# Optimization experiments

Measured on AMD Instinct MI355X. Metric: run time of the kernel, lower is better.

The kernel has to match this reference:

```python
import jax, jax.numpy as jnp
import numpy as np

T, B, OBS, A, P, NB, H = 32, 256, 1024, 16, 600, 601, 128


def setup_inputs() -> dict:
    key = jax.random.key(0)
    ks = jax.random.split(key, 32)
    f32 = jnp.float32

    def rn(k, shape, scale):
        return jax.random.normal(k, shape, dtype=f32) * scale

    hh = 1.0 / np.sqrt(H)
    inp = {
        "obs_seq": rn(ks[0], (T, B, OBS), 1.0),
        # backbone MLP (512, 512)
        "bb_w1": rn(ks[1], (OBS, 512), 1.0 / np.sqrt(OBS)), "bb_b1": jnp.zeros((512,), f32),
        "bb_w2": rn(ks[2], (512, 512), 1.0 / np.sqrt(512)), "bb_b2": jnp.zeros((512,), f32),
        # feedforward heads (final layers init std=0.01, bias 0 per module)
        "pol_w": rn(ks[3], (512, A), 0.01), "pol_b": jnp.zeros((A,), f32),
        "y_w": rn(ks[4], (512, P), 0.01), "y_b": jnp.zeros((P,), f32),
        "ci_w": rn(ks[5], (512, H), 1.0 / np.sqrt(512)), "ci_b": jnp.zeros((H,), f32),
        # LSTMCell(A, 128): gate order i,f,g,o as in torch
        "w_ih": rn(ks[6], (A, 4 * H), hh), "w_hh": rn(ks[7], (H, 4 * H), hh),
        "b_ih": rn(ks[8], (4 * H,), hh), "b_hh": rn(ks[9], (4 * H,), hh),
        # z / q / aux_pi MLPs: Linear(128,128) -> ReLU -> Linear(128, out)
        "z_w1": rn(ks[10], (H, H), hh), "z_b1": jnp.zeros((H,), f32),
        "z_w2": rn(ks[11], (H, P), 0.01), "z_b2": jnp.zeros((P,), f32),
        "q_w1": rn(ks[12], (H, H), hh), "q_b1": jnp.zeros((H,), f32),
        "q_w2": rn(ks[13], (H, NB), 0.01), "q_b2": jnp.zeros((NB,), f32),
        "a_w1": rn(ks[14], (H, H), hh), "a_b1": jnp.zeros((H,), f32),
        "a_w2": rn(ks[15], (H, A), 0.01), "a_b2": jnp.zeros((A,), f32),
    }
    return inp


def reference(obs_seq, bb_w1, bb_b1, bb_w2, bb_b2, pol_w, pol_b, y_w, y_b,
              ci_w, ci_b, w_ih, w_hh, b_ih, b_hh,
              z_w1, z_b1, z_w2, z_b2, q_w1, q_b1, q_w2, q_b2,
              a_w1, a_b1, a_w2, a_b2):
    Tn, Bn = obs_seq.shape[:2]
    x = obs_seq.reshape(Tn * Bn, -1)  # feedforward across time: fold T into batch
    emb = jax.nn.relu(jax.nn.relu(x @ bb_w1 + bb_b1) @ bb_w2 + bb_b2)  # [N,512]
    logits = emb @ pol_w + pol_b  # [N,A]
    y = emb @ y_w + y_b           # [N,P]
    c0 = emb @ ci_w + ci_b        # [N,H]
    h0 = jnp.tanh(c0)

    # one_hot(a) @ W_ih^T == row a of W_ih (input-to-gate contribution per action)
    in_gates = w_ih + b_ih  # [A, 4H]

    def step(carry, ig):
        h, c = carry
        g = ig + h @ w_hh + b_hh  # [N,4H]
        i, f, gg, o = jnp.split(g, 4, axis=-1)  # torch gate order i,f,g,o
        c = jax.nn.sigmoid(f) * c + jax.nn.sigmoid(i) * jnp.tanh(gg)
        h = jax.nn.sigmoid(o) * jnp.tanh(c)
        return (h, c), h

    _, h_all = jax.lax.scan(step, (h0, c0), in_gates)  # [A, N, H]

    def mlp(hx, w1, b1, w2, b2):
        return jax.nn.relu(hx @ w1 + b1) @ w2 + b2

    def to_tba(arr):
        Aa, N, D = arr.shape
        return arr.reshape(Aa, Tn, Bn, D).transpose(1, 2, 0, 3)  # [T,B,A,D]

    z = to_tba(mlp(h_all, z_w1, z_b1, z_w2, z_b2))
    q = to_tba(mlp(h_all, q_w1, q_b1, q_w2, q_b2))
    aux_pi = to_tba(mlp(h_all, a_w1, a_b1, a_w2, a_b2))
    return (logits.reshape(Tn, Bn, -1), y.reshape(Tn, Bn, -1), z, q, aux_pi)
```

## Files before the change

### kernel.cpp

```cpp
#include <hip/hip_runtime.h>
#include <stdint.h>

typedef short bf16x8 __attribute__((ext_vector_type(8)));
typedef float f32x4 __attribute__((ext_vector_type(4)));

__device__ __forceinline__ unsigned short f2b(float f) {
  union { float f; unsigned u; } v; v.f = f;
  unsigned r = v.u + 0x7fffu + ((v.u >> 16) & 1u);
  return (unsigned short)(r >> 16);
}

struct TD { const float* in; unsigned short* out; int R, C; };
struct TDs { TD d[12]; };

__global__ __launch_bounds__(256) void tconv_all(TDs ds) {
  TD t = ds.d[blockIdx.z];
  int c0 = blockIdx.x * 32, r0 = blockIdx.y * 32;
  if (c0 >= t.C || r0 >= t.R) return;
  __shared__ float tl[32][33];
  int tx = threadIdx.x & 31, ty = threadIdx.x >> 5;
  #pragma unroll
  for (int i = 0; i < 32; i += 8) {
    int r = r0 + ty + i, c = c0 + tx;
    tl[ty + i][tx] = (r < t.R && c < t.C) ? t.in[(size_t)r * t.C + c] : 0.f;
  }
  __syncthreads();
  #pragma unroll
  for (int i = 0; i < 32; i += 8) {
    int c = c0 + ty + i, r = r0 + tx;
    if (c < t.C && r < t.R) t.out[(size_t)c * t.R + r] = f2b(tl[tx][ty + i]);
  }
}

__global__ __launch_bounds__(256) void conv_k(const float* __restrict__ in,
                                              unsigned short* __restrict__ out, int n) {
  int i = (blockIdx.x * 256 + threadIdx.x) * 8;
  if (i >= n) return;
  float4 a = *(const float4*)(in + i);
  float4 b = *(const float4*)(in + i + 4);
  bf16x8 v;
  v[0] = (short)f2b(a.x); v[1] = (short)f2b(a.y); v[2] = (short)f2b(a.z); v[3] = (short)f2b(a.w);
  v[4] = (short)f2b(b.x); v[5] = (short)f2b(b.y); v[6] = (short)f2b(b.z); v[7] = (short)f2b(b.w);
  *(bf16x8*)(out + i) = v;
}

template <int ACT, bool OBF16>
__global__ __launch_bounds__(256) void gemm_k(const unsigned short* __restrict__ A,
                                              const unsigned short* __restrict__ BT,
                                              const float* __restrict__ bias,
                                              void* __restrict__ Cp,
                                              int M, int N, int K, int ldC) {
  __shared__ unsigned short As[64][40];
  __shared__ unsigned short Bs[64][40];
  const int tid = threadIdx.x;
  const int n0 = blockIdx.x * 64;
  const int m0 = blockIdx.y * 64;
  const int wid = tid >> 6, lane = tid & 63;
  const int wm = (wid >> 1) * 32, wn = (wid & 1) * 32;
  const int lr = lane & 15, lk = lane >> 4;
  const int sr = tid >> 2, sc = (tid & 3) * 8;

  f32x4 acc[2][2] = {};

  for (int k0 = 0; k0 < K; k0 += 32) {
    *(bf16x8*)&As[sr][sc] = *(const bf16x8*)(A + (size_t)(m0 + sr) * K + k0 + sc);
    {
      int n = n0 + sr;
      bf16x8 v = {};
      if (n < N) v = *(const bf16x8*)(BT + (size_t)n * K + k0 + sc);
      *(bf16x8*)&Bs[sr][sc] = v;
    }
    __syncthreads();
    bf16x8 af[2], bfr[2];
    #pragma unroll
    for (int mi = 0; mi < 2; mi++) af[mi] = *(const bf16x8*)&As[wm + mi * 16 + lr][lk * 8];
    #pragma unroll
    for (int ni = 0; ni < 2; ni++) bfr[ni] = *(const bf16x8*)&Bs[wn + ni * 16 + lr][lk * 8];
    #pragma unroll
    for (int mi = 0; mi < 2; mi++)
      #pragma unroll
      for (int ni = 0; ni < 2; ni++)
        acc[mi][ni] = __builtin_amdgcn_mfma_f32_16x16x32_bf16(af[mi], bfr[ni], acc[mi][ni], 0, 0, 0);
    __syncthreads();
  }

  #pragma unroll
  for (int mi = 0; mi < 2; mi++)
    #pragma unroll
    for (int ni = 0; ni < 2; ni++) {
      int col = n0 + wn + ni * 16 + lr;
      if (col >= N) continue;
      float bv = bias[col];
      #pragma unroll
      for (int r = 0; r < 4; r++) {
        int row = m0 + wm + mi * 16 + lk * 4 + r;
        float v = acc[mi][ni][r] + bv;
        if (ACT == 1) v = fmaxf(v, 0.f);
        if (OBF16) ((unsigned short*)Cp)[(size_t)row * ldC + col] = f2b(v);
        else       ((float*)Cp)[(size_t)row * ldC + col] = v;
      }
    }
}

__global__ __launch_bounds__(256) void lstm_k(const float* __restrict__ c0,
                                              const unsigned short* __restrict__ whhT,
                                              const float* __restrict__ w_ih,
                                              const float* __restrict__ b_ih,
                                              const float* __restrict__ b_hh,
                                              unsigned short* __restrict__ h_all) {
  __shared__ float G[32][516];
  __shared__ float cst[32][128];
  __shared__ unsigned short hst[32][136];
  const int tid = threadIdx.x, lane = tid & 63, wid = tid >> 6;
  const int r0 = blockIdx.x * 32;
  const int lr = lane & 15, lk = lane >> 4;

  for (int e = tid; e < 32 * 128; e += 256) {
    int r = e >> 7, j = e & 127;
    float c = c0[(size_t)(r0 + r) * 128 + j];
    cst[r][j] = c;
    hst[r][j] = f2b(tanhf(c));
  }
  __syncthreads();

  for (int a = 0; a < 16; a++) {
    f32x4 acc[2][8] = {};
    #pragma unroll
    for (int ks = 0; ks < 4; ks++) {
      bf16x8 af0 = *(const bf16x8*)&hst[lr][ks * 32 + lk * 8];
      bf16x8 af1 = *(const bf16x8*)&hst[16 + lr][ks * 32 + lk * 8];
      #pragma unroll
      for (int ni = 0; ni < 8; ni++) {
        int col = wid * 128 + ni * 16 + lr;
        bf16x8 bv = *(const bf16x8*)(whhT + (size_t)col * 128 + ks * 32 + lk * 8);
        acc[0][ni] = __builtin_amdgcn_mfma_f32_16x16x32_bf16(af0, bv, acc[0][ni], 0, 0, 0);
        acc[1][ni] = __builtin_amdgcn_mfma_f32_16x16x32_bf16(af1, bv, acc[1][ni], 0, 0, 0);
      }
    }
    #pragma unroll
    for (int mi = 0; mi < 2; mi++)
      #pragma unroll
      for (int ni = 0; ni < 8; ni++)
        #pragma unroll
        for (int rr = 0; rr < 4; rr++)
          G[mi * 16 + lk * 4 + rr][wid * 128 + ni * 16 + lr] = acc[mi][ni][rr];
    __syncthreads();

    const float* ig = w_ih + a * 512;
    for (int e = tid; e < 32 * 128; e += 256) {
      int r = e >> 7, j = e & 127;
      float gi = G[r][j]       + ig[j]       + b_ih[j]       + b_hh[j];
      float gf = G[r][j + 128] + ig[j + 128] + b_ih[j + 128] + b_hh[j + 128];
      float gg = G[r][j + 256] + ig[j + 256] + b_ih[j + 256] + b_hh[j + 256];
      float go = G[r][j + 384] + ig[j + 384] + b_ih[j + 384] + b_hh[j + 384];
      float c = cst[r][j];
      float si = 1.f / (1.f + __expf(-gi));
      float sf = 1.f / (1.f + __expf(-gf));
      float so = 1.f / (1.f + __expf(-go));
      float cn = sf * c + si * tanhf(gg);
      float h = so * tanhf(cn);
      cst[r][j] = cn;
      unsigned short hb = f2b(h);
      hst[r][j] = hb;
      h_all[((size_t)(r0 + r) * 16 + a) * 128 + j] = hb;
    }
    __syncthreads();
  }
}

__global__ __launch_bounds__(256) void heads_k(
    const unsigned short* __restrict__ hall,
    const unsigned short* __restrict__ zw1, const float* __restrict__ zb1,
    const unsigned short* __restrict__ zw2, const float* __restrict__ zb2,
    const unsigned short* __restrict__ qw1, const float* __restrict__ qb1,
    const unsigned short* __restrict__ qw2, const float* __restrict__ qb2,
    const unsigned short* __restrict__ aw1, const float* __restrict__ ab1,
    const unsigned short* __restrict__ aw2, const float* __restrict__ ab2,
    float* __restrict__ oz, float* __restrict__ oq, float* __restrict__ oa) {
  __shared__ unsigned short hs[64][136];
  __shared__ unsigned short hd[64][136];
  const int tid = threadIdx.x;
  const int r0 = blockIdx.x * 64;
  const int lane = tid & 63, wid = tid >> 6;
  const int lr = lane & 15, lk = lane >> 4;

  {
    int row = tid >> 2, cb = (tid & 3) * 8;
    #pragma unroll
    for (int it = 0; it < 4; it++) {
      int col = cb + it * 32;
      *(bf16x8*)&hs[row][col] = *(const bf16x8*)(hall + (size_t)(r0 + row) * 128 + col);
    }
  }
  __syncthreads();

  const unsigned short* W1[3] = {zw1, qw1, aw1};
  const float*          B1[3] = {zb1, qb1, ab1};
  const unsigned short* W2[3] = {zw2, qw2, aw2};
  const float*          B2[3] = {zb2, qb2, ab2};
  float*                OO[3] = {oz, oq, oa};
  const int             NN[3] = {600, 601, 16};

  #pragma unroll
  for (int hi = 0; hi < 3; hi++) {
    const unsigned short* w1 = W1[hi];
    const unsigned short* w2 = W2[hi];
    const float* b1 = B1[hi];
    const float* b2 = B2[hi];
    float* Oh = OO[hi];
    const int Nh = NN[hi];

    {
      bf16x8 ha[4][4];
      #pragma unroll
      for (int mi = 0; mi < 4; mi++)
        #pragma unroll
        for (int ks = 0; ks < 4; ks++)
          ha[mi][ks] = *(const bf16x8*)&hs[mi * 16 + lr][ks * 32 + lk * 8];
      f32x4 hacc[4][2] = {};
      #pragma unroll
      for (int ks = 0; ks < 4; ks++)
        #pragma unroll
        for (int nj = 0; nj < 2; nj++) {
          int col = wid * 32 + nj * 16 + lr;
          bf16x8 bv = *(const bf16x8*)(w1 + (size_t)col * 128 + ks * 32 + lk * 8);
          #pragma unroll
          for (int mi = 0; mi < 4; mi++)
            hacc[mi][nj] = __builtin_amdgcn_mfma_f32_16x16x32_bf16(ha[mi][ks], bv, hacc[mi][nj], 0, 0, 0);
        }
      #pragma unroll
      for (int mi = 0; mi < 4; mi++)
        #pragma unroll
        for (int nj = 0; nj < 2; nj++) {
          int col = wid * 32 + nj * 16 + lr;
          float bb = b1[col];
          #pragma unroll
          for (int rr = 0; rr < 4; rr++) {
            int row = mi * 16 + lk * 4 + rr;
            hd[row][col] = f2b(fmaxf(hacc[mi][nj][rr] + bb, 0.f));
          }
        }
    }
    __syncthreads();

    {
      bf16x8 hda[4][4];
      #pragma unroll
      for (int mi = 0; mi < 4; mi++)
        #pragma unroll
        for (int ks = 0; ks < 4; ks++)
          hda[mi][ks] = *(const bf16x8*)&hd[mi * 16 + lr][ks * 32 + lk * 8];

      const int NF = (Nh + 15) >> 4;
      const int fpw = (NF + 3) >> 2;
      const int f0 = wid * fpw;
      const int f1 = min(NF, f0 + fpw);

      for (int f = f0; f < f1; f += 2) {
        f32x4 oacc[4][2] = {};
        #pragma unroll
        for (int ks = 0; ks < 4; ks++)
          #pragma unroll
          for (int nj = 0; nj < 2; nj++) {
            int nf = f + nj; nf = nf < f1 ? nf : f1 - 1;
            int col = nf * 16 + lr;
            int bc = col < Nh ? col : Nh - 1;
            bf16x8 bv = *(const bf16x8*)(w2 + (size_t)bc * 128 + ks * 32 + lk * 8);
            #pragma unroll
            for (int mi = 0; mi < 4; mi++)
              oacc[mi][nj] = __builtin_amdgcn_mfma_f32_16x16x32_bf16(hda[mi][ks], bv, oacc[mi][nj], 0, 0, 0);
          }
        #pragma unroll
        for (int nj = 0; nj < 2; nj++) {
          int nf = f + nj;
          if (nf >= f1) break;
          int col = nf * 16 + lr;
          if (col < Nh) {
            float bb = b2[col];
            #pragma unroll
            for (int mi = 0; mi < 4; mi++)
              #pragma unroll
              for (int rr = 0; rr < 4; rr++) {
                int row = r0 + mi * 16 + lk * 4 + rr;
                Oh[(size_t)row * Nh + col] = oacc[mi][nj][rr] + bb;
              }
          }
        }
      }
    }
    __syncthreads();
  }
}

extern "C" void kernel_launch(void* const* d_in, const int* in_sizes, int n_in,
                              void* d_out, int out_size, void* d_ws, size_t ws_size,
                              hipStream_t stream) {
  const float* obs   = (const float*)d_in[0];
  const float* bb_w1 = (const float*)d_in[1];
  const float* bb_b1 = (const float*)d_in[2];
  const float* bb_w2 = (const float*)d_in[3];
  const float* bb_b2 = (const float*)d_in[4];
  const float* pol_w = (const float*)d_in[5];
  const float* pol_b = (const float*)d_in[6];
  const float* y_w   = (const float*)d_in[7];
  const float* y_b   = (const float*)d_in[8];
  const float* ci_w  = (const float*)d_in[9];
  const float* ci_b  = (const float*)d_in[10];
  const float* w_ih  = (const float*)d_in[11];
  const float* w_hh  = (const float*)d_in[12];
  const float* b_ih  = (const float*)d_in[13];
  const float* b_hh  = (const float*)d_in[14];
  const float* z_w1  = (const float*)d_in[15];
  const float* z_b1  = (const float*)d_in[16];
  const float* z_w2  = (const float*)d_in[17];
  const float* z_b2  = (const float*)d_in[18];
  const float* q_w1  = (const float*)d_in[19];
  const float* q_b1  = (const float*)d_in[20];
  const float* q_w2  = (const float*)d_in[21];
  const float* q_b2  = (const float*)d_in[22];
  const float* a_w1  = (const float*)d_in[23];
  const float* a_b1  = (const float*)d_in[24];
  const float* a_w2  = (const float*)d_in[25];
  const float* a_b2  = (const float*)d_in[26];

  float* out = (float*)d_out;
  float* out_logits = out;
  float* out_y      = out + 131072;
  float* out_z      = out + 5046272;
  float* out_q      = out + 83689472;
  float* out_a      = out + 162463744;

  uint8_t* ws = (uint8_t*)d_ws;
  size_t off = 0;
  auto alc = [&](size_t bytes) -> void* {
    void* p = ws + off;
    off = (off + bytes + 255) & ~(size_t)255;
    return p;
  };
  unsigned short* W1T  = (unsigned short*)alc((size_t)512 * 1024 * 2);
  unsigned short* W2T  = (unsigned short*)alc((size_t)512 * 512 * 2);
  unsigned short* polT = (unsigned short*)alc((size_t)16 * 512 * 2);
  unsigned short* yT   = (unsigned short*)alc((size_t)600 * 512 * 2);
  unsigned short* ciT  = (unsigned short*)alc((size_t)128 * 512 * 2);
  unsigned short* whhT = (unsigned short*)alc((size_t)512 * 128 * 2);
  unsigned short* zw1T = (unsigned short*)alc((size_t)128 * 128 * 2);
  unsigned short* zw2T = (unsigned short*)alc((size_t)600 * 128 * 2);
  unsigned short* qw1T = (unsigned short*)alc((size_t)128 * 128 * 2);
  unsigned short* qw2T = (unsigned short*)alc((size_t)601 * 128 * 2);
  unsigned short* aw1T = (unsigned short*)alc((size_t)128 * 128 * 2);
  unsigned short* aw2T = (unsigned short*)alc((size_t)16 * 128 * 2);
  unsigned short* obsb = (unsigned short*)alc((size_t)8192 * 1024 * 2);
  unsigned short* hid1 = (unsigned short*)alc((size_t)8192 * 512 * 2);
  unsigned short* emb  = (unsigned short*)alc((size_t)8192 * 512 * 2);
  float*          c0b  = (float*)alc((size_t)8192 * 128 * 4);
  unsigned short* hall = (unsigned short*)alc((size_t)8192 * 16 * 128 * 2);
  (void)ws_size; (void)in_sizes; (void)n_in; (void)out_size;

  dim3 B256(256);

  TDs td;
  td.d[0]  = {bb_w1, W1T, 1024, 512};
  td.d[1]  = {bb_w2, W2T, 512, 512};
  td.d[2]  = {pol_w, polT, 512, 16};
  td.d[3]  = {y_w,   yT,   512, 600};
  td.d[4]  = {ci_w,  ciT,  512, 128};
  td.d[5]  = {w_hh,  whhT, 128, 512};
  td.d[6]  = {z_w1,  zw1T, 128, 128};
  td.d[7]  = {z_w2,  zw2T, 128, 600};
  td.d[8]  = {q_w1,  qw1T, 128, 128};
  td.d[9]  = {q_w2,  qw2T, 128, 601};
  td.d[10] = {a_w1,  aw1T, 128, 128};
  td.d[11] = {a_w2,  aw2T, 128, 16};
  tconv_all<<<dim3(19, 32, 12), B256, 0, stream>>>(td);

  conv_k<<<dim3(4096), B256, 0, stream>>>(obs, obsb, 8192 * 1024);

  gemm_k<1, true><<<dim3(8, 128), B256, 0, stream>>>(obsb, W1T, bb_b1, hid1, 8192, 512, 1024, 512);
  gemm_k<1, true><<<dim3(8, 128), B256, 0, stream>>>(hid1, W2T, bb_b2, emb,  8192, 512, 512,  512);
  gemm_k<0, false><<<dim3(1, 128),  B256, 0, stream>>>(emb, polT, pol_b, out_logits, 8192, 16,  512, 16);
  gemm_k<0, false><<<dim3(10, 128), B256, 0, stream>>>(emb, yT,   y_b,   out_y,      8192, 600, 512, 600);
  gemm_k<0, false><<<dim3(2, 128),  B256, 0, stream>>>(emb, ciT,  ci_b,  c0b,        8192, 128, 512, 128);
  lstm_k<<<dim3(256), B256, 0, stream>>>(c0b, whhT, w_ih, b_ih, b_hh, hall);
  heads_k<<<dim3(2048), B256, 0, stream>>>(hall,
                                           zw1T, z_b1, zw2T, z_b2,
                                           qw1T, q_b1, qw2T, q_b2,
                                           aw1T, a_b1, aw2T, a_b2,
                                           out_z, out_q, out_a);
}
```

Before: 523.2 us.

## Widen LSTM blocks, fuse head first layers, use nontemporal output stores

```diff
diff --git a/kernel.cpp b/kernel.cpp
--- a/kernel.cpp
+++ b/kernel.cpp
@@ -3,11 +3,18 @@
 
 typedef short bf16x8 __attribute__((ext_vector_type(8)));
 typedef float f32x4 __attribute__((ext_vector_type(4)));
+typedef unsigned short u16x4 __attribute__((ext_vector_type(4)));
 
 __device__ __forceinline__ unsigned short f2b(float f) {
   union { float f; unsigned u; } v; v.f = f;
   unsigned r = v.u + 0x7fffu + ((v.u >> 16) & 1u);
   return (unsigned short)(r >> 16);
+}
+__device__ __forceinline__ float fsigm(float x) { return 1.f / (1.f + __expf(-x)); }
+__device__ __forceinline__ float ftanh(float x) {
+  float t = __expf(-2.f * fabsf(x));
+  float r = (1.f - t) / (1.f + t);
+  return copysignf(r, x);
 }
 
 struct TD { const float* in; unsigned short* out; int R, C; };
@@ -44,7 +51,7 @@
   *(bf16x8*)(out + i) = v;
 }
 
-template <int ACT, bool OBF16>
+template <int ACT, bool OBF16, bool NT>
 __global__ __launch_bounds__(256) void gemm_k(const unsigned short* __restrict__ A,
                                               const unsigned short* __restrict__ BT,
                                               const float* __restrict__ bias,
@@ -97,17 +104,18 @@
         float v = acc[mi][ni][r] + bv;
         if (ACT == 1) v = fmaxf(v, 0.f);
         if (OBF16) ((unsigned short*)Cp)[(size_t)row * ldC + col] = f2b(v);
+        else if (NT) __builtin_nontemporal_store(v, (float*)Cp + (size_t)row * ldC + col);
         else       ((float*)Cp)[(size_t)row * ldC + col] = v;
       }
     }
 }
 
-__global__ __launch_bounds__(256) void lstm_k(const float* __restrict__ c0,
-                                              const unsigned short* __restrict__ whhT,
-                                              const float* __restrict__ w_ih,
-                                              const float* __restrict__ b_ih,
-                                              const float* __restrict__ b_hh,
-                                              unsigned short* __restrict__ h_all) {
+__global__ __launch_bounds__(1024) void lstm_k(const float* __restrict__ c0,
+                                               const unsigned short* __restrict__ whhT,
+                                               const float* __restrict__ w_ih,
+                                               const float* __restrict__ b_ih,
+                                               const float* __restrict__ b_hh,
+                                               unsigned short* __restrict__ h_all) {
   __shared__ float G[32][516];
   __shared__ float cst[32][128];
   __shared__ unsigned short hst[32][136];
@@ -115,50 +123,52 @@
   const int r0 = blockIdx.x * 32;
   const int lr = lane & 15, lk = lane >> 4;
 
-  for (int e = tid; e < 32 * 128; e += 256) {
-    int r = e >> 7, j = e & 127;
-    float c = c0[(size_t)(r0 + r) * 128 + j];
-    cst[r][j] = c;
-    hst[r][j] = f2b(tanhf(c));
+  {
+    int r = tid >> 5, j4 = (tid & 31) * 4;
+    float4 c4 = *(const float4*)(c0 + (size_t)(r0 + r) * 128 + j4);
+    *(f32x4*)&cst[r][j4] = f32x4{c4.x, c4.y, c4.z, c4.w};
+    u16x4 h4;
+    h4[0] = f2b(ftanh(c4.x)); h4[1] = f2b(ftanh(c4.y));
+    h4[2] = f2b(ftanh(c4.z)); h4[3] = f2b(ftanh(c4.w));
+    *(u16x4*)&hst[r][j4] = h4;
   }
   __syncthreads();
 
   for (int a = 0; a < 16; a++) {
-    f32x4 acc[2][8] = {};
+    f32x4 acc[2][2] = {};
     #pragma unroll
     for (int ks = 0; ks < 4; ks++) {
       bf16x8 af0 = *(const bf16x8*)&hst[lr][ks * 32 + lk * 8];
       bf16x8 af1 = *(const bf16x8*)&hst[16 + lr][ks * 32 + lk * 8];
       #pragma unroll
-      for (int ni = 0; ni < 8; ni++) {
-        int col = wid * 128 + ni * 16 + lr;
+      for (int nj = 0; nj < 2; nj++) {
+        int col = wid * 32 + nj * 16 + lr;
         bf16x8 bv = *(const bf16x8*)(whhT + (size_t)col * 128 + ks * 32 + lk * 8);
-        acc[0][ni] = __builtin_amdgcn_mfma_f32_16x16x32_bf16(af0, bv, acc[0][ni], 0, 0, 0);
-        acc[1][ni] = __builtin_amdgcn_mfma_f32_16x16x32_bf16(af1, bv, acc[1][ni], 0, 0, 0);
+        acc[0][nj] = __builtin_amdgcn_mfma_f32_16x16x32_bf16(af0, bv, acc[0][nj], 0, 0, 0);
+        acc[1][nj] = __builtin_amdgcn_mfma_f32_16x16x32_bf16(af1, bv, acc[1][nj], 0, 0, 0);
       }
     }
     #pragma unroll
     for (int mi = 0; mi < 2; mi++)
       #pragma unroll
-      for (int ni = 0; ni < 8; ni++)
+      for (int nj = 0; nj < 2; nj++)
         #pragma unroll
         for (int rr = 0; rr < 4; rr++)
-          G[mi * 16 + lk * 4 + rr][wid * 128 + ni * 16 + lr] = acc[mi][ni][rr];
+          G[mi * 16 + lk * 4 + rr][wid * 32 + nj * 16 + lr] = acc[mi][nj][rr];
     __syncthreads();
 
     const float* ig = w_ih + a * 512;
-    for (int e = tid; e < 32 * 128; e += 256) {
+    #pragma unroll
+    for (int it = 0; it < 4; it++) {
+      int e = tid + it * 1024;
       int r = e >> 7, j = e & 127;
       float gi = G[r][j]       + ig[j]       + b_ih[j]       + b_hh[j];
       float gf = G[r][j + 128] + ig[j + 128] + b_ih[j + 128] + b_hh[j + 128];
       float gg = G[r][j + 256] + ig[j + 256] + b_ih[j + 256] + b_hh[j + 256];
       float go = G[r][j + 384] + ig[j + 384] + b_ih[j + 384] + b_hh[j + 384];
       float c = cst[r][j];
-      float si = 1.f / (1.f + __expf(-gi));
-      float sf = 1.f / (1.f + __expf(-gf));
-      float so = 1.f / (1.f + __expf(-go));
-      float cn = sf * c + si * tanhf(gg);
-      float h = so * tanhf(cn);
+      float cn = fsigm(gf) * c + fsigm(gi) * ftanh(gg);
+      float h = fsigm(go) * ftanh(cn);
       cst[r][j] = cn;
       unsigned short hb = f2b(h);
       hst[r][j] = hb;
@@ -170,15 +180,13 @@
 
 __global__ __launch_bounds__(256) void heads_k(
     const unsigned short* __restrict__ hall,
-    const unsigned short* __restrict__ zw1, const float* __restrict__ zb1,
-    const unsigned short* __restrict__ zw2, const float* __restrict__ zb2,
-    const unsigned short* __restrict__ qw1, const float* __restrict__ qb1,
-    const unsigned short* __restrict__ qw2, const float* __restrict__ qb2,
-    const unsigned short* __restrict__ aw1, const float* __restrict__ ab1,
-    const unsigned short* __restrict__ aw2, const float* __restrict__ ab2,
+    const unsigned short* __restrict__ w1cat,
+    const float* __restrict__ zb1, const float* __restrict__ qb1, const float* __restrict__ ab1,
+    const unsigned short* __restrict__ w2cat,
+    const float* __restrict__ zb2, const float* __restrict__ qb2, const float* __restrict__ ab2,
     float* __restrict__ oz, float* __restrict__ oq, float* __restrict__ oa) {
   __shared__ unsigned short hs[64][136];
-  __shared__ unsigned short hd[64][136];
+  __shared__ unsigned short hd[64][392];
   const int tid = threadIdx.x;
   const int r0 = blockIdx.x * 64;
   const int lane = tid & 63, wid = tid >> 6;
@@ -194,101 +202,75 @@
   }
   __syncthreads();
 
-  const unsigned short* W1[3] = {zw1, qw1, aw1};
-  const float*          B1[3] = {zb1, qb1, ab1};
-  const unsigned short* W2[3] = {zw2, qw2, aw2};
-  const float*          B2[3] = {zb2, qb2, ab2};
-  float*                OO[3] = {oz, oq, oa};
-  const int             NN[3] = {600, 601, 16};
+  {
+    bf16x8 ha[4][4];
+    #pragma unroll
+    for (int mi = 0; mi < 4; mi++)
+      #pragma unroll
+      for (int ks = 0; ks < 4; ks++)
+        ha[mi][ks] = *(const bf16x8*)&hs[mi * 16 + lr][ks * 32 + lk * 8];
+    #pragma unroll
+    for (int j = 0; j < 6; j++) {
+      int nf = wid * 6 + j;
+      int col = nf * 16 + lr;
+      bf16x8 bv[4];
+      #pragma unroll
+      for (int ks = 0; ks < 4; ks++)
+        bv[ks] = *(const bf16x8*)(w1cat + (size_t)col * 128 + ks * 32 + lk * 8);
+      f32x4 hacc[4] = {};
+      #pragma unroll
+      for (int ks = 0; ks < 4; ks++)
+        #pragma unroll
+        for (int mi = 0; mi < 4; mi++)
+          hacc[mi] = __builtin_amdgcn_mfma_f32_16x16x32_bf16(ha[mi][ks], bv[ks], hacc[mi], 0, 0, 0);
+      float bb = (col < 128) ? zb1[col] : (col < 256) ? qb1[col - 128] : ab1[col - 256];
+      #pragma unroll
+      for (int mi = 0; mi < 4; mi++)
+        #pragma unroll
+        for (int rr = 0; rr < 4; rr++)
+          hd[mi * 16 + lk * 4 + rr][col] = f2b(fmaxf(hacc[mi][rr] + bb, 0.f));
+    }
+  }
+  __syncthreads();
 
   #pragma unroll
   for (int hi = 0; hi < 3; hi++) {
-    const unsigned short* w1 = W1[hi];
-    const unsigned short* w2 = W2[hi];
-    const float* b1 = B1[hi];
-    const float* b2 = B2[hi];
-    float* Oh = OO[hi];
-    const int Nh = NN[hi];
-
-    {
-      bf16x8 ha[4][4];
-      #pragma unroll
-      for (int mi = 0; mi < 4; mi++)
-        #pragma unroll
-        for (int ks = 0; ks < 4; ks++)
-          ha[mi][ks] = *(const bf16x8*)&hs[mi * 16 + lr][ks * 32 + lk * 8];
-      f32x4 hacc[4][2] = {};
-      #pragma unroll
-      for (int ks = 0; ks < 4; ks++)
-        #pragma unroll
-        for (int nj = 0; nj < 2; nj++) {
-          int col = wid * 32 + nj * 16 + lr;
-          bf16x8 bv = *(const bf16x8*)(w1 + (size_t)col * 128 + ks * 32 + lk * 8);
+    const int NF = (hi == 0) ? 38 : (hi == 1) ? 38 : 1;
+    const int Nh = (hi == 0) ? 600 : (hi == 1) ? 601 : 16;
+    const int so = (hi == 0) ? 0 : (hi == 1) ? 600 : 1201;
+    const float* b2 = (hi == 0) ? zb2 : (hi == 1) ? qb2 : ab2;
+    float* Oh = (hi == 0) ? oz : (hi == 1) ? oq : oa;
+
+    bf16x8 hda[4][4];
+    #pragma unroll
+    for (int mi = 0; mi < 4; mi++)
+      #pragma unroll
+      for (int ks = 0; ks < 4; ks++)
+        hda[mi][ks] = *(const bf16x8*)&hd[mi * 16 + lr][hi * 128 + ks * 32 + lk * 8];
+
+    for (int f = wid; f < NF; f += 4) {
+      int col = f * 16 + lr;
+      int bc = col < Nh ? col : Nh - 1;
+      bf16x8 bv[4];
+      #pragma unroll
+      for (int ks = 0; ks < 4; ks++)
+        bv[ks] = *(const bf16x8*)(w2cat + (size_t)(so + bc) * 128 + ks * 32 + lk * 8);
+      f32x4 oacc[4] = {};
+      #pragma unroll
+      for (int ks = 0; ks < 4; ks++)
+        #pragma unroll
+        for (int mi = 0; mi < 4; mi++)
+          oacc[mi] = __builtin_amdgcn_mfma_f32_16x16x32_bf16(hda[mi][ks], bv[ks], oacc[mi], 0, 0, 0);
+      if (col < Nh) {
+        float bb = b2[col];
+        #pragma unroll
+        for (int mi = 0; mi < 4; mi++)
           #pragma unroll
-          for (int mi = 0; mi < 4; mi++)
-            hacc[mi][nj] = __builtin_amdgcn_mfma_f32_16x16x32_bf16(ha[mi][ks], bv, hacc[mi][nj], 0, 0, 0);
-        }
-      #pragma unroll
-      for (int mi = 0; mi < 4; mi++)
-        #pragma unroll
-        for (int nj = 0; nj < 2; nj++) {
-          int col = wid * 32 + nj * 16 + lr;
-          float bb = b1[col];
-          #pragma unroll
-          for (int rr = 0; rr < 4; rr++) {
-            int row = mi * 16 + lk * 4 + rr;
-            hd[row][col] = f2b(fmaxf(hacc[mi][nj][rr] + bb, 0.f));
-          }
-        }
-    }
-    __syncthreads();
-
-    {
-      bf16x8 hda[4][4];
-      #pragma unroll
-      for (int mi = 0; mi < 4; mi++)
-        #pragma unroll
-        for (int ks = 0; ks < 4; ks++)
-          hda[mi][ks] = *(const bf16x8*)&hd[mi * 16 + lr][ks * 32 + lk * 8];
-
-      const int NF = (Nh + 15) >> 4;
-      const int fpw = (NF + 3) >> 2;
-      const int f0 = wid * fpw;
-      const int f1 = min(NF, f0 + fpw);
-
-      for (int f = f0; f < f1; f += 2) {
-        f32x4 oacc[4][2] = {};
-        #pragma unroll
-        for (int ks = 0; ks < 4; ks++)
-          #pragma unroll
-          for (int nj = 0; nj < 2; nj++) {
-            int nf = f + nj; nf = nf < f1 ? nf : f1 - 1;
-            int col = nf * 16 + lr;
-            int bc = col < Nh ? col : Nh - 1;
-            bf16x8 bv = *(const bf16x8*)(w2 + (size_t)bc * 128 + ks * 32 + lk * 8);
-            #pragma unroll
-            for (int mi = 0; mi < 4; mi++)
-              oacc[mi][nj] = __builtin_amdgcn_mfma_f32_16x16x32_bf16(hda[mi][ks], bv, oacc[mi][nj], 0, 0, 0);
-          }
-        #pragma unroll
-        for (int nj = 0; nj < 2; nj++) {
-          int nf = f + nj;
-          if (nf >= f1) break;
-          int col = nf * 16 + lr;
-          if (col < Nh) {
-            float bb = b2[col];
-            #pragma unroll
-            for (int mi = 0; mi < 4; mi++)
-              #pragma unroll
-              for (int rr = 0; rr < 4; rr++) {
-                int row = r0 + mi * 16 + lk * 4 + rr;
-                Oh[(size_t)row * Nh + col] = oacc[mi][nj][rr] + bb;
-              }
-          }
-        }
+          for (int rr = 0; rr < 4; rr++)
+            __builtin_nontemporal_store(oacc[mi][rr] + bb,
+                Oh + (size_t)(r0 + mi * 16 + lk * 4 + rr) * Nh + col);
       }
     }
-    __syncthreads();
   }
 }
 
@@ -344,10 +326,10 @@
   unsigned short* ciT  = (unsigned short*)alc((size_t)128 * 512 * 2);
   unsigned short* whhT = (unsigned short*)alc((size_t)512 * 128 * 2);
   unsigned short* zw1T = (unsigned short*)alc((size_t)128 * 128 * 2);
+  unsigned short* qw1T = (unsigned short*)alc((size_t)128 * 128 * 2);
+  unsigned short* aw1T = (unsigned short*)alc((size_t)128 * 128 * 2);
   unsigned short* zw2T = (unsigned short*)alc((size_t)600 * 128 * 2);
-  unsigned short* qw1T = (unsigned short*)alc((size_t)128 * 128 * 2);
   unsigned short* qw2T = (unsigned short*)alc((size_t)601 * 128 * 2);
-  unsigned short* aw1T = (unsigned short*)alc((size_t)128 * 128 * 2);
   unsigned short* aw2T = (unsigned short*)alc((size_t)16 * 128 * 2);
   unsigned short* obsb = (unsigned short*)alc((size_t)8192 * 1024 * 2);
   unsigned short* hid1 = (unsigned short*)alc((size_t)8192 * 512 * 2);
@@ -375,15 +357,14 @@
 
   conv_k<<<dim3(4096), B256, 0, stream>>>(obs, obsb, 8192 * 1024);
 
-  gemm_k<1, true><<<dim3(8, 128), B256, 0, stream>>>(obsb, W1T, bb_b1, hid1, 8192, 512, 1024, 512);
-  gemm_k<1, true><<<dim3(8, 128), B256, 0, stream>>>(hid1, W2T, bb_b2, emb,  8192, 512, 512,  512);
-  gemm_k<0, false><<<dim3(1, 128),  B256, 0, stream>>>(emb, polT, pol_b, out_logits, 8192, 16,  512, 16);
-  gemm_k<0, false><<<dim3(10, 128), B256, 0, stream>>>(emb, yT,   y_b,   out_y,      8192, 600, 512, 600);
-  gemm_k<0, false><<<dim3(2, 128),  B256, 0, stream>>>(emb, ciT,  ci_b,  c0b,        8192, 128, 512, 128);
-  lstm_k<<<dim3(256), B256, 0, stream>>>(c0b, whhT, w_ih, b_ih, b_hh, hall);
+  gemm_k<1, true,  false><<<dim3(8, 128), B256, 0, stream>>>(obsb, W1T, bb_b1, hid1, 8192, 512, 1024, 512);
+  gemm_k<1, true,  false><<<dim3(8, 128), B256, 0, stream>>>(hid1, W2T, bb_b2, emb,  8192, 512, 512,  512);
+  gemm_k<0, false, true><<<dim3(1, 128),  B256, 0, stream>>>(emb, polT, pol_b, out_logits, 8192, 16,  512, 16);
+  gemm_k<0, false, true><<<dim3(10, 128), B256, 0, stream>>>(emb, yT,   y_b,   out_y,      8192, 600, 512, 600);
+  gemm_k<0, false, false><<<dim3(2, 128), B256, 0, stream>>>(emb, ciT,  ci_b,  c0b,        8192, 128, 512, 128);
+  lstm_k<<<dim3(256), dim3(1024), 0, stream>>>(c0b, whhT, w_ih, b_ih, b_hh, hall);
   heads_k<<<dim3(2048), B256, 0, stream>>>(hall,
-                                           zw1T, z_b1, zw2T, z_b2,
-                                           qw1T, q_b1, qw2T, q_b2,
-                                           aw1T, a_b1, aw2T, a_b2,
+                                           zw1T, z_b1, q_b1, a_b1,
+                                           zw2T, z_b2, q_b2, a_b2,
                                            out_z, out_q, out_a);
 }
```

Measured after the change: 777.0 us. 48.5% more time.
